# Optimization experiments

Hardware: AMD Instinct MI355X
Metric: run time of the kernel (lower is better)

## Reference

```python
import jax, jax.numpy as jnp
import numpy as np

ROI = 7
EPS = 1e-3


def roi_align(images, frame_idx, boxes_px, oh, ow):
    """Bilinear RoIAlign, sampling_ratio=1 (bin centers), aligned=False.
    images: [F,C,H,W]; frame_idx: [R] int; boxes_px: [R,4] pixel coords.
    Returns [R,oh,ow,C]."""
    F_, C, H, W = images.shape
    R = boxes_px.shape[0]
    x1, y1, x2, y2 = (boxes_px[:, i] for i in range(4))
    bw = (x2 - x1) / ow
    bh = (y2 - y1) / oh
    sx = x1[:, None] + (jnp.arange(ow, dtype=boxes_px.dtype) + 0.5) * bw[:, None]  # [R,ow]
    sy = y1[:, None] + (jnp.arange(oh, dtype=boxes_px.dtype) + 0.5) * bh[:, None]  # [R,oh]
    X = jnp.broadcast_to(sx[:, None, :], (R, oh, ow))
    Y = jnp.broadcast_to(sy[:, :, None], (R, oh, ow))
    valid = (X > -1.0) & (X < W) & (Y > -1.0) & (Y < H)
    x = jnp.clip(X, 0.0, W - 1)
    y = jnp.clip(Y, 0.0, H - 1)
    x0 = jnp.floor(x).astype(jnp.int32)
    y0 = jnp.floor(y).astype(jnp.int32)
    x1i = jnp.minimum(x0 + 1, W - 1)
    y1i = jnp.minimum(y0 + 1, H - 1)
    lx = x - x0
    ly = y - y0
    f = frame_idx[:, None, None]

    def g(yy, xx):
        return images[f, :, yy, xx]  # [R,oh,ow,C]

    v = (g(y0, x0) * ((1 - ly) * (1 - lx))[..., None]
         + g(y0, x1i) * ((1 - ly) * lx)[..., None]
         + g(y1i, x0) * (ly * (1 - lx))[..., None]
         + g(y1i, x1i) * (ly * lx)[..., None])
    return v * valid[..., None].astype(v.dtype)


def bn(x, gamma, beta, mean, var):
    return (x - mean) * jax.lax.rsqrt(var + EPS) * gamma + beta


def setup_inputs() -> dict:
    key = jax.random.key(0)
    ks = jax.random.split(key, 12)
    F_, C, H, W = 64, 256, 40, 40
    N, K = 512, 8
    HID, D = 512, 512
    images = jax.random.normal(ks[0], (F_, C, H, W), jnp.float32)
    kf_indices = jax.random.randint(ks[1], (N, K), 0, F_, jnp.int32)
    u = jax.random.uniform(ks[2], (N, K, 4), jnp.float32)
    x1 = u[..., 0] * 0.6
    y1 = u[..., 1] * 0.6
    x2 = jnp.minimum(x1 + 0.2 + u[..., 2] * 0.2, 1.0)
    y2 = jnp.minimum(y1 + 0.2 + u[..., 3] * 0.2, 1.0)
    boxes = jnp.stack([x1, y1, x2, y2], axis=-1)
    fan1 = C * ROI * ROI
    w1 = jax.random.normal(ks[3], (HID, C, ROI, ROI), jnp.float32) * np.float32(np.sqrt(2.0 / fan1))
    b1 = jnp.zeros((HID,), jnp.float32)
    w2 = jax.random.normal(ks[4], (D, HID), jnp.float32) * np.float32(np.sqrt(2.0 / HID))
    b2 = jnp.zeros((D,), jnp.float32)
    g1 = jnp.ones((HID,), jnp.float32)
    bt1 = jnp.zeros((HID,), jnp.float32)
    m1 = jax.random.normal(ks[5], (HID,), jnp.float32) * 0.1
    v1 = 0.5 + jax.random.uniform(ks[6], (HID,), jnp.float32)
    g2 = jnp.ones((D,), jnp.float32)
    bt2 = jnp.zeros((D,), jnp.float32)
    m2 = jax.random.normal(ks[7], (D,), jnp.float32) * 0.1
    v2 = 0.5 + jax.random.uniform(ks[8], (D,), jnp.float32)
    return {"images": images, "kf_indices": kf_indices, "boxes": boxes,
            "w1": w1, "b1": b1, "g1": g1, "bt1": bt1, "m1": m1, "v1": v1,
            "w2": w2, "b2": b2, "g2": g2, "bt2": bt2, "m2": m2, "v2": v2}


def reference(images, kf_indices, boxes, w1, b1, g1, bt1, m1, v1, w2, b2, g2, bt2, m2, v2):
    F_, C, H, W = images.shape
    N, K = kf_indices.shape
    scale = jnp.asarray([W, H, W, H], images.dtype)
    boxes_px = (boxes * scale).reshape(N * K, 4)
    fidx = kf_indices.reshape(-1)
    roi = roi_align(images, fidx, boxes_px, ROI, ROI)        # [R,7,7,C]
    # conv1 with kernel == roi_region collapses spatial dims -> dense GEMM
    h = jnp.einsum('rhwc,ochw->ro', roi, w1) + b1            # [R,HID]
    h = jax.nn.relu(bn(h, g1, bt1, m1, v1))
    h = h @ w2.T + b2                                        # [R,D]
    h = jax.nn.relu(bn(h, g2, bt2, m2, v2))
    nodes = jnp.max(h.reshape(N, K, -1), axis=1)             # max-aggr over keyframes
    return nodes
```

## Files before the change

kernel.cpp:

```cpp
#include <hip/hip_runtime.h>


typedef __bf16 bf16x8 __attribute__((ext_vector_type(8)));
typedef float f32x4 __attribute__((ext_vector_type(4)));
typedef ushort us8v __attribute__((ext_vector_type(8)));

#define BN_EPS 1e-3f

__device__ __forceinline__ ushort f2bf(float f) {
  union { float f; unsigned u; } v; v.f = f;
  unsigned r = (v.u + 0x7FFFu + ((v.u >> 16) & 1u)) >> 16;
  return (ushort)r;
}
__device__ __forceinline__ float bf2f(ushort b) {
  union { unsigned u; float f; } v; v.u = ((unsigned)b) << 16;
  return v.f;
}
__device__ __forceinline__ void async16(const void* g, void* l) {
  __builtin_amdgcn_global_load_lds((const __attribute__((address_space(1))) void*)g,
                                   (__attribute__((address_space(3))) void*)l, 16, 0, 0);
}

__global__ __launch_bounds__(256, 6) void prep_kernel(const float* __restrict__ img,
                                                      ushort* __restrict__ imgTb,
                                                      const float* __restrict__ w1,
                                                      ushort* __restrict__ w1b,
                                                      const float* __restrict__ w2,
                                                      ushort* __restrict__ w2b,
                                                      const int* __restrict__ kf,
                                                      int* __restrict__ perm) {
  __shared__ __align__(16) char smem[26368];
  const int b = blockIdx.x;
  const int tid = threadIdx.x;
  int tIdx = -1, oIdx = -1;
  if (b < 2307) {
    int q = b / 3, r = b - q * 3;
    if (r < 2) tIdx = q * 2 + r; else oIdx = q;
  } else {
    tIdx = 1538 + (b - 2307);
  }
  if (tIdx >= 0) {
    ushort* lds = (ushort*)smem;
    const int f = tIdx >> 5, rem = tIdx & 31;
    const int cg = rem >> 2, ps = rem & 3;
    const float* src = img + (size_t)f * 409600 + (size_t)(cg * 32) * 1600 + ps * 400;
    for (int i = tid; i < 3200; i += 256) {
      int ch = i / 100, pos = i - ch * 100;
      float4 v = *(const float4*)(src + (size_t)ch * 1600 + pos * 4);
      ushort4 o;
      o.x = f2bf(v.x); o.y = f2bf(v.y); o.z = f2bf(v.z); o.w = f2bf(v.w);
      *(ushort4*)(&lds[ch * 412 + pos * 4]) = o;
    }
    __syncthreads();
    ushort* dst = imgTb + ((size_t)f * 1600 + ps * 400) * 256 + cg * 32;
    for (int e = tid; e < 1600; e += 256) {
      int p = e >> 2, q = e & 3;
      us8v o;
#pragma unroll
      for (int k = 0; k < 8; ++k) o[k] = lds[(q * 8 + k) * 412 + p];
      *(us8v*)(dst + (size_t)p * 256 + q * 8) = o;
    }
  } else if (oIdx < 512) {
    ushort* t = (ushort*)smem;
    const int o = oIdx;
    const float* src = w1 + (size_t)o * 12544;
    for (int j = tid; j < 12544; j += 256) {
      int c = j / 49, p = j - c * 49;
      t[p * 260 + c] = f2bf(src[j]);
    }
    __syncthreads();
    ushort* dst = w1b + (size_t)o * 12544;
    for (int k0 = tid * 8; k0 < 12544; k0 += 2048) {
      int p = k0 >> 8, c = k0 & 255;
      ushort4 a = *(const ushort4*)(&t[p * 260 + c]);
      ushort4 d = *(const ushort4*)(&t[p * 260 + c + 4]);
      us8v o8;
      o8[0] = a.x; o8[1] = a.y; o8[2] = a.z; o8[3] = a.w;
      o8[4] = d.x; o8[5] = d.y; o8[6] = d.z; o8[7] = d.w;
      *(us8v*)(dst + k0) = o8;
    }
  } else if (oIdx < 768) {
    const int o2 = oIdx - 512;
    const size_t base = (size_t)o2 * 1024 + tid * 4;
    float4 vv = *(const float4*)(w2 + base);
    ushort4 o4;
    o4.x = f2bf(vv.x); o4.y = f2bf(vv.y); o4.z = f2bf(vv.z); o4.w = f2bf(vv.w);
    *(ushort4*)(w2b + base) = o4;
  } else {
    int* cnt = (int*)smem;
    int* base = cnt + 64;
    if (tid < 64) cnt[tid] = 0;
    __syncthreads();
    for (int r = tid; r < 4096; r += 256) atomicAdd(&cnt[kf[r]], 1);
    __syncthreads();
    if (tid == 0) {
      int acc = 0;
      for (int f = 0; f < 64; ++f) { base[f] = acc; acc += cnt[f]; }
    }
    __syncthreads();
    for (int r = tid; r < 4096; r += 256) {
      int p = atomicAdd(&base[kf[r]], 1);
      perm[p] = r;
    }
  }
}

__global__ __launch_bounds__(256) void roi_kernel(const ushort* __restrict__ imgTb,
                                                  const int* __restrict__ kf,
                                                  const float* __restrict__ boxes,
                                                  const int* __restrict__ perm,
                                                  ushort* __restrict__ A) {
  __shared__ int sy0[49], sx0[49], sy1[49], sx1[49];
  __shared__ float sw00[49], sw01[49], sw10[49], sw11[49];
  __shared__ int sf, sr;
  const int tid = threadIdx.x;
  if (tid == 0) {
    int r = perm[((blockIdx.x & 7) << 9) | (blockIdx.x >> 3)];
    sr = r;
    sf = kf[r];
  }
  __syncthreads();
  const int r = sr;
  if (tid < 49) {
    int py = tid / 7, px = tid % 7;
    float x1 = boxes[r * 4 + 0] * 40.f, y1 = boxes[r * 4 + 1] * 40.f;
    float x2 = boxes[r * 4 + 2] * 40.f, y2 = boxes[r * 4 + 3] * 40.f;
    float bw = (x2 - x1) * (1.f / 7.f), bh = (y2 - y1) * (1.f / 7.f);
    float X = x1 + (px + 0.5f) * bw, Y = y1 + (py + 0.5f) * bh;
    bool valid = (X > -1.f) && (X < 40.f) && (Y > -1.f) && (Y < 40.f);
    float x = fminf(fmaxf(X, 0.f), 39.f), y = fminf(fmaxf(Y, 0.f), 39.f);
    float x0f = floorf(x), y0f = floorf(y);
    int x0 = (int)x0f, y0 = (int)y0f;
    int x1i = min(x0 + 1, 39), y1i = min(y0 + 1, 39);
    float lx = x - x0f, ly = y - y0f;
    float vm = valid ? 1.f : 0.f;
    sx0[tid] = x0; sy0[tid] = y0; sx1[tid] = x1i; sy1[tid] = y1i;
    sw00[tid] = (1.f - ly) * (1.f - lx) * vm;
    sw01[tid] = (1.f - ly) * lx * vm;
    sw10[tid] = ly * (1.f - lx) * vm;
    sw11[tid] = ly * lx * vm;
  }
  __syncthreads();
  const int c8 = (tid & 31) * 8;
  const int pq = tid >> 5;
  const ushort* base = imgTb + (size_t)sf * 409600 + c8;
  ushort* outp = A + (size_t)r * 12544 + c8;
  for (int p = pq; p < 49; p += 8) {
    const us8v a = *(const us8v*)(base + (size_t)(sy0[p] * 40 + sx0[p]) * 256);
    const us8v b = *(const us8v*)(base + (size_t)(sy0[p] * 40 + sx1[p]) * 256);
    const us8v c = *(const us8v*)(base + (size_t)(sy1[p] * 40 + sx0[p]) * 256);
    const us8v d = *(const us8v*)(base + (size_t)(sy1[p] * 40 + sx1[p]) * 256);
    float w00 = sw00[p], w01 = sw01[p], w10 = sw10[p], w11 = sw11[p];
    us8v o;
#pragma unroll
    for (int k = 0; k < 8; ++k)
      o[k] = f2bf(bf2f(a[k]) * w00 + bf2f(b[k]) * w01 + bf2f(c[k]) * w10 + bf2f(d[k]) * w11);
    *(us8v*)(outp + (size_t)p * 256) = o;
  }
}

__global__ __launch_bounds__(256, 4) void gemm1_kernel(const ushort* __restrict__ A,
                                                       const ushort* __restrict__ B,
                                                       ushort* __restrict__ P) {
  constexpr int K = 12544;
  constexpr int KS = 1792;
  __shared__ __align__(16) ushort sA[128 * 64];
  __shared__ __align__(16) ushort sB[128 * 64];
  const int tid = threadIdx.x;
  const int lane = tid & 63, wave = tid >> 6;
  const int wm = wave >> 1, wn = wave & 1;
  const int r16 = lane & 15, quad = lane >> 4;
  const int r0 = blockIdx.x * 128, c0 = blockIdx.y * 128;
  const int kStart = blockIdx.z * KS, kEnd = kStart + KS;
  const ushort* Ab = A + (size_t)r0 * K;
  const ushort* Bb = B + (size_t)c0 * K;
  const int row8 = tid >> 3;
  const int koff = (((tid & 7) ^ (row8 & 7))) * 8;
  const int sw = r16 & 7;
  f32x4 acc[4][4] = {};
  for (int kk = kStart; kk < kEnd; kk += 64) {
    __syncthreads();
#pragma unroll
    for (int s = 0; s < 4; ++s)
      async16(Ab + (size_t)(s * 32 + row8) * K + kk + koff, (char*)sA + s * 4096 + tid * 16);
#pragma unroll
    for (int s = 0; s < 4; ++s)
      async16(Bb + (size_t)(s * 32 + row8) * K + kk + koff, (char*)sB + s * 4096 + tid * 16);
    __syncthreads();
#pragma unroll
    for (int h = 0; h < 2; ++h) {
      const int slot = ((h * 4 + quad) ^ sw) * 8;
      bf16x8 af[4], bfr[4];
#pragma unroll
      for (int i = 0; i < 4; ++i)
        af[i] = *(const bf16x8*)(sA + (wm * 64 + i * 16 + r16) * 64 + slot);
#pragma unroll
      for (int j = 0; j < 4; ++j)
        bfr[j] = *(const bf16x8*)(sB + (wn * 64 + j * 16 + r16) * 64 + slot);
#pragma unroll
      for (int i = 0; i < 4; ++i)
#pragma unroll
        for (int j = 0; j < 4; ++j)
          acc[i][j] = __builtin_amdgcn_mfma_f32_16x16x32_bf16(af[i], bfr[j], acc[i][j], 0, 0, 0);
    }
  }
  ushort* Pz = P + ((size_t)blockIdx.z * 4096 + r0) * 512 + c0;
#pragma unroll
  for (int i = 0; i < 4; ++i)
#pragma unroll
    for (int j = 0; j < 4; ++j)
#pragma unroll
      for (int g = 0; g < 4; ++g)
        Pz[(size_t)(wm * 64 + i * 16 + quad * 4 + g) * 512 + (wn * 64 + j * 16 + r16)] =
            f2bf(acc[i][j][g]);
}

__global__ __launch_bounds__(256) void combine_kernel(const ushort* __restrict__ P,
                                                      const float* __restrict__ b1,
                                                      const float* __restrict__ g1,
                                                      const float* __restrict__ bt1,
                                                      const float* __restrict__ m1,
                                                      const float* __restrict__ v1,
                                                      ushort* __restrict__ h1) {
  size_t i = (size_t)blockIdx.x * 256 + threadIdx.x;
  int col = (int)(i & 511);
  float x = 0.f;
#pragma unroll
  for (int z = 0; z < 7; ++z) x += bf2f(P[i + (size_t)z * 2097152]);
  float s = g1[col] * rsqrtf(v1[col] + BN_EPS);
  float val = fmaxf((x + b1[col] - m1[col]) * s + bt1[col], 0.f);
  h1[i] = f2bf(val);
}

__global__ __launch_bounds__(256) void gemm2_kernel(const ushort* __restrict__ A,
                                                    const ushort* __restrict__ B,
                                                    const float* __restrict__ b2,
                                                    const float* __restrict__ g2,
                                                    const float* __restrict__ bt2,
                                                    const float* __restrict__ m2,
                                                    const float* __restrict__ v2,
                                                    float* __restrict__ out) {
  constexpr int K = 512;
  __shared__ __align__(16) ushort sA[64 * 64];
  __shared__ __align__(16) ushort sB[128 * 64];
  __shared__ ushort st[64 * 128];
  const int tid = threadIdx.x;
  const int lane = tid & 63, wave = tid >> 6;
  const int wm = wave >> 1, wn = wave & 1;
  const int r16 = lane & 15, quad = lane >> 4;
  const int r0 = blockIdx.x * 64, c0 = blockIdx.y * 128;
  const ushort* Ab = A + (size_t)r0 * K;
  const ushort* Bb = B + (size_t)c0 * K;
  const int row8 = tid >> 3;
  const int koff = (((tid & 7) ^ (row8 & 7))) * 8;
  const int sw = r16 & 7;
  f32x4 acc[2][4] = {};
  for (int kk = 0; kk < K; kk += 64) {
    __syncthreads();
#pragma unroll
    for (int s = 0; s < 2; ++s)
      async16(Ab + (size_t)(s * 32 + row8) * K + kk + koff, (char*)sA + s * 4096 + tid * 16);
#pragma unroll
    for (int s = 0; s < 4; ++s)
      async16(Bb + (size_t)(s * 32 + row8) * K + kk + koff, (char*)sB + s * 4096 + tid * 16);
    __syncthreads();
#pragma unroll
    for (int h = 0; h < 2; ++h) {
      const int slot = ((h * 4 + quad) ^ sw) * 8;
      bf16x8 af[2], bfr[4];
#pragma unroll
      for (int i = 0; i < 2; ++i)
        af[i] = *(const bf16x8*)(sA + (wm * 32 + i * 16 + r16) * 64 + slot);
#pragma unroll
      for (int j = 0; j < 4; ++j)
        bfr[j] = *(const bf16x8*)(sB + (wn * 64 + j * 16 + r16) * 64 + slot);
#pragma unroll
      for (int i = 0; i < 2; ++i)
#pragma unroll
        for (int j = 0; j < 4; ++j)
          acc[i][j] = __builtin_amdgcn_mfma_f32_16x16x32_bf16(af[i], bfr[j], acc[i][j], 0, 0, 0);
    }
  }
  float ss[4], tt[4], bbv[4];
#pragma unroll
  for (int j = 0; j < 4; ++j) {
    int c = c0 + wn * 64 + j * 16 + r16;
    float s = g2[c] * rsqrtf(v2[c] + BN_EPS);
    ss[j] = s; tt[j] = bt2[c] - m2[c] * s; bbv[j] = b2[c];
  }
#pragma unroll
  for (int i = 0; i < 2; ++i)
#pragma unroll
    for (int j = 0; j < 4; ++j)
#pragma unroll
      for (int g = 0; g < 4; ++g) {
        int rr = wm * 32 + i * 16 + quad * 4 + g;
        int cc = wn * 64 + j * 16 + r16;
        float x = (acc[i][j][g] + bbv[j]) * ss[j] + tt[j];
        st[rr * 128 + cc] = f2bf(fmaxf(x, 0.f));
      }
  __syncthreads();
  for (int e = tid; e < 1024; e += 256) {
    int gg = e >> 7, cc = e & 127;
    float m = 0.f;
#pragma unroll
    for (int k = 0; k < 8; ++k) m = fmaxf(m, bf2f(st[(gg * 8 + k) * 128 + cc]));
    out[(size_t)(r0 / 8 + gg) * 512 + c0 + cc] = m;
  }
}

extern "C" void kernel_launch(void* const* d_in, const int* in_sizes, int n_in,
                              void* d_out, int out_size, void* d_ws, size_t ws_size,
                              hipStream_t stream) {
  (void)in_sizes; (void)n_in; (void)out_size; (void)ws_size;
  const float* images = (const float*)d_in[0];
  const int* kf      = (const int*)d_in[1];
  const float* boxes = (const float*)d_in[2];
  const float* w1    = (const float*)d_in[3];
  const float* b1    = (const float*)d_in[4];
  const float* g1    = (const float*)d_in[5];
  const float* bt1   = (const float*)d_in[6];
  const float* m1    = (const float*)d_in[7];
  const float* v1    = (const float*)d_in[8];
  const float* w2    = (const float*)d_in[9];
  const float* b2    = (const float*)d_in[10];
  const float* g2    = (const float*)d_in[11];
  const float* bt2   = (const float*)d_in[12];
  const float* m2    = (const float*)d_in[13];
  const float* v2    = (const float*)d_in[14];
  float* out = (float*)d_out;

  char* ws = (char*)d_ws;
  ushort* Abuf  = (ushort*)(ws + 0);
  ushort* w1b   = (ushort*)(ws + 102760448);
  ushort* w2b   = (ushort*)(ws + 115605504);
  ushort* imgTb = (ushort*)(ws + 116129792);
  ushort* P     = (ushort*)(ws + 116129792);
  ushort* h1    = (ushort*)(ws + 149684224);
  int*    perm  = (int*)(ws + 168558592);

  hipLaunchKernelGGL(prep_kernel, dim3(2817), dim3(256), 0, stream,
                     images, imgTb, w1, w1b, w2, w2b, kf, perm);
  hipLaunchKernelGGL(roi_kernel, dim3(4096), dim3(256), 0, stream, imgTb, kf, boxes, perm, Abuf);
  hipLaunchKernelGGL(gemm1_kernel, dim3(32, 4, 7), dim3(256), 0, stream, Abuf, w1b, P);
  hipLaunchKernelGGL(combine_kernel, dim3(8192), dim3(256), 0, stream, P, b1, g1, bt1, m1, v1, h1);
  hipLaunchKernelGGL(gemm2_kernel, dim3(64, 4), dim3(256), 0, stream, h1, w2b, b2, g2, bt2, m2, v2, out);
}
```

Measured before the change: 324.7 us.

## Fuse image bf16 conversion into RoIAlign with per-frame LDS-resident channel slices

```diff
diff --git a/kernel.cpp b/kernel.cpp
--- a/kernel.cpp
+++ b/kernel.cpp
@@ -21,55 +21,25 @@
                                    (__attribute__((address_space(3))) void*)l, 16, 0, 0);
 }
 
-__global__ __launch_bounds__(256, 6) void prep_kernel(const float* __restrict__ img,
-                                                      ushort* __restrict__ imgTb,
-                                                      const float* __restrict__ w1,
-                                                      ushort* __restrict__ w1b,
-                                                      const float* __restrict__ w2,
-                                                      ushort* __restrict__ w2b,
-                                                      const int* __restrict__ kf,
-                                                      int* __restrict__ perm) {
-  __shared__ __align__(16) char smem[26368];
+__global__ __launch_bounds__(256) void prep_kernel(const float* __restrict__ w1,
+                                                   ushort* __restrict__ w1b,
+                                                   const float* __restrict__ w2,
+                                                   ushort* __restrict__ w2b,
+                                                   const int* __restrict__ kf,
+                                                   int* __restrict__ perm,
+                                                   int* __restrict__ fstart) {
+  __shared__ __align__(16) char smem[25480];
   const int b = blockIdx.x;
   const int tid = threadIdx.x;
-  int tIdx = -1, oIdx = -1;
-  if (b < 2307) {
-    int q = b / 3, r = b - q * 3;
-    if (r < 2) tIdx = q * 2 + r; else oIdx = q;
-  } else {
-    tIdx = 1538 + (b - 2307);
-  }
-  if (tIdx >= 0) {
-    ushort* lds = (ushort*)smem;
-    const int f = tIdx >> 5, rem = tIdx & 31;
-    const int cg = rem >> 2, ps = rem & 3;
-    const float* src = img + (size_t)f * 409600 + (size_t)(cg * 32) * 1600 + ps * 400;
-    for (int i = tid; i < 3200; i += 256) {
-      int ch = i / 100, pos = i - ch * 100;
-      float4 v = *(const float4*)(src + (size_t)ch * 1600 + pos * 4);
-      ushort4 o;
-      o.x = f2bf(v.x); o.y = f2bf(v.y); o.z = f2bf(v.z); o.w = f2bf(v.w);
-      *(ushort4*)(&lds[ch * 412 + pos * 4]) = o;
-    }
-    __syncthreads();
-    ushort* dst = imgTb + ((size_t)f * 1600 + ps * 400) * 256 + cg * 32;
-    for (int e = tid; e < 1600; e += 256) {
-      int p = e >> 2, q = e & 3;
-      us8v o;
-#pragma unroll
-      for (int k = 0; k < 8; ++k) o[k] = lds[(q * 8 + k) * 412 + p];
-      *(us8v*)(dst + (size_t)p * 256 + q * 8) = o;
-    }
-  } else if (oIdx < 512) {
+  if (b < 512) {
     ushort* t = (ushort*)smem;
-    const int o = oIdx;
-    const float* src = w1 + (size_t)o * 12544;
+    const float* src = w1 + (size_t)b * 12544;
     for (int j = tid; j < 12544; j += 256) {
       int c = j / 49, p = j - c * 49;
       t[p * 260 + c] = f2bf(src[j]);
     }
     __syncthreads();
-    ushort* dst = w1b + (size_t)o * 12544;
+    ushort* dst = w1b + (size_t)b * 12544;
     for (int k0 = tid * 8; k0 < 12544; k0 += 2048) {
       int p = k0 >> 8, c = k0 & 255;
       ushort4 a = *(const ushort4*)(&t[p * 260 + c]);
@@ -79,8 +49,8 @@
       o8[4] = d.x; o8[5] = d.y; o8[6] = d.z; o8[7] = d.w;
       *(us8v*)(dst + k0) = o8;
     }
-  } else if (oIdx < 768) {
-    const int o2 = oIdx - 512;
+  } else if (b < 768) {
+    const int o2 = b - 512;
     const size_t base = (size_t)o2 * 1024 + tid * 4;
     float4 vv = *(const float4*)(w2 + base);
     ushort4 o4;
@@ -95,7 +65,8 @@
     __syncthreads();
     if (tid == 0) {
       int acc = 0;
-      for (int f = 0; f < 64; ++f) { base[f] = acc; acc += cnt[f]; }
+      for (int f = 0; f < 64; ++f) { base[f] = acc; fstart[f] = acc; acc += cnt[f]; }
+      fstart[64] = acc;
     }
     __syncthreads();
     for (int r = tid; r < 4096; r += 256) {
@@ -105,57 +76,53 @@
   }
 }
 
-__global__ __launch_bounds__(256) void roi_kernel(const ushort* __restrict__ imgTb,
-                                                  const int* __restrict__ kf,
-                                                  const float* __restrict__ boxes,
-                                                  const int* __restrict__ perm,
-                                                  ushort* __restrict__ A) {
-  __shared__ int sy0[49], sx0[49], sy1[49], sx1[49];
-  __shared__ float sw00[49], sw01[49], sw10[49], sw11[49];
-  __shared__ int sf, sr;
+__global__ __launch_bounds__(512) void roi_fused_kernel(const float* __restrict__ img,
+                                                        const float* __restrict__ boxes,
+                                                        const int* __restrict__ perm,
+                                                        const int* __restrict__ fstart,
+                                                        ushort* __restrict__ A) {
+  __shared__ ushort lds[32 * 1604];
   const int tid = threadIdx.x;
-  if (tid == 0) {
-    int r = perm[((blockIdx.x & 7) << 9) | (blockIdx.x >> 3)];
-    sr = r;
-    sf = kf[r];
+  const int f = blockIdx.x >> 3, cg = blockIdx.x & 7;
+  const float* src = img + (size_t)f * 409600 + (size_t)(cg * 32) * 1600;
+  for (int i = tid; i < 12800; i += 512) {
+    int ch = i / 400, pos = i - ch * 400;
+    float4 v = *(const float4*)(src + (size_t)ch * 1600 + pos * 4);
+    ushort4 o;
+    o.x = f2bf(v.x); o.y = f2bf(v.y); o.z = f2bf(v.z); o.w = f2bf(v.w);
+    *(ushort4*)(&lds[ch * 1604 + pos * 4]) = o;
   }
   __syncthreads();
-  const int r = sr;
-  if (tid < 49) {
-    int py = tid / 7, px = tid % 7;
-    float x1 = boxes[r * 4 + 0] * 40.f, y1 = boxes[r * 4 + 1] * 40.f;
-    float x2 = boxes[r * 4 + 2] * 40.f, y2 = boxes[r * 4 + 3] * 40.f;
-    float bw = (x2 - x1) * (1.f / 7.f), bh = (y2 - y1) * (1.f / 7.f);
-    float X = x1 + (px + 0.5f) * bw, Y = y1 + (py + 0.5f) * bh;
-    bool valid = (X > -1.f) && (X < 40.f) && (Y > -1.f) && (Y < 40.f);
-    float x = fminf(fmaxf(X, 0.f), 39.f), y = fminf(fmaxf(Y, 0.f), 39.f);
-    float x0f = floorf(x), y0f = floorf(y);
-    int x0 = (int)x0f, y0 = (int)y0f;
-    int x1i = min(x0 + 1, 39), y1i = min(y0 + 1, 39);
-    float lx = x - x0f, ly = y - y0f;
-    float vm = valid ? 1.f : 0.f;
-    sx0[tid] = x0; sy0[tid] = y0; sx1[tid] = x1i; sy1[tid] = y1i;
-    sw00[tid] = (1.f - ly) * (1.f - lx) * vm;
-    sw01[tid] = (1.f - ly) * lx * vm;
-    sw10[tid] = ly * (1.f - lx) * vm;
-    sw11[tid] = ly * lx * vm;
-  }
-  __syncthreads();
-  const int c8 = (tid & 31) * 8;
-  const int pq = tid >> 5;
-  const ushort* base = imgTb + (size_t)sf * 409600 + c8;
-  ushort* outp = A + (size_t)r * 12544 + c8;
-  for (int p = pq; p < 49; p += 8) {
-    const us8v a = *(const us8v*)(base + (size_t)(sy0[p] * 40 + sx0[p]) * 256);
-    const us8v b = *(const us8v*)(base + (size_t)(sy0[p] * 40 + sx1[p]) * 256);
-    const us8v c = *(const us8v*)(base + (size_t)(sy1[p] * 40 + sx0[p]) * 256);
-    const us8v d = *(const us8v*)(base + (size_t)(sy1[p] * 40 + sx1[p]) * 256);
-    float w00 = sw00[p], w01 = sw01[p], w10 = sw10[p], w11 = sw11[p];
-    us8v o;
-#pragma unroll
-    for (int k = 0; k < 8; ++k)
-      o[k] = f2bf(bf2f(a[k]) * w00 + bf2f(b[k]) * w01 + bf2f(c[k]) * w10 + bf2f(d[k]) * w11);
-    *(us8v*)(outp + (size_t)p * 256) = o;
+  const int s0 = fstart[f], s1 = fstart[f + 1];
+  ushort* Abase = A + cg * 32;
+  for (int idx = s0; idx < s1; ++idx) {
+    const int r = perm[idx];
+    const float bx1 = boxes[r * 4 + 0] * 40.f, by1 = boxes[r * 4 + 1] * 40.f;
+    const float bx2 = boxes[r * 4 + 2] * 40.f, by2 = boxes[r * 4 + 3] * 40.f;
+    const float bw = (bx2 - bx1) * (1.f / 7.f), bh = (by2 - by1) * (1.f / 7.f);
+    ushort* outp = Abase + (size_t)r * 12544;
+    for (int it = tid; it < 1568; it += 512) {
+      const int p = it >> 5, ch = it & 31;
+      const int py = p / 7, px = p - py * 7;
+      const float X = bx1 + (px + 0.5f) * bw, Y = by1 + (py + 0.5f) * bh;
+      const bool valid = (X > -1.f) && (X < 40.f) && (Y > -1.f) && (Y < 40.f);
+      const float x = fminf(fmaxf(X, 0.f), 39.f), y = fminf(fmaxf(Y, 0.f), 39.f);
+      const float x0f = floorf(x), y0f = floorf(y);
+      const int x0 = (int)x0f, y0 = (int)y0f;
+      const int x1i = min(x0 + 1, 39), y1i = min(y0 + 1, 39);
+      const float lx = x - x0f, ly = y - y0f;
+      const float vm = valid ? 1.f : 0.f;
+      const float w00 = (1.f - ly) * (1.f - lx) * vm;
+      const float w01 = (1.f - ly) * lx * vm;
+      const float w10 = ly * (1.f - lx) * vm;
+      const float w11 = ly * lx * vm;
+      const ushort* row = &lds[ch * 1604];
+      const float a = bf2f(row[y0 * 40 + x0]);
+      const float b = bf2f(row[y0 * 40 + x1i]);
+      const float c = bf2f(row[y1i * 40 + x0]);
+      const float d = bf2f(row[y1i * 40 + x1i]);
+      outp[p * 256 + ch] = f2bf(a * w00 + b * w01 + c * w10 + d * w11);
+    }
   }
 }
 
@@ -334,14 +301,15 @@
   ushort* Abuf  = (ushort*)(ws + 0);
   ushort* w1b   = (ushort*)(ws + 102760448);
   ushort* w2b   = (ushort*)(ws + 115605504);
-  ushort* imgTb = (ushort*)(ws + 116129792);
   ushort* P     = (ushort*)(ws + 116129792);
   ushort* h1    = (ushort*)(ws + 149684224);
   int*    perm  = (int*)(ws + 168558592);
-
-  hipLaunchKernelGGL(prep_kernel, dim3(2817), dim3(256), 0, stream,
-                     images, imgTb, w1, w1b, w2, w2b, kf, perm);
-  hipLaunchKernelGGL(roi_kernel, dim3(4096), dim3(256), 0, stream, imgTb, kf, boxes, perm, Abuf);
+  int*    fstart= (int*)(ws + 168574976);
+
+  hipLaunchKernelGGL(prep_kernel, dim3(769), dim3(256), 0, stream,
+                     w1, w1b, w2, w2b, kf, perm, fstart);
+  hipLaunchKernelGGL(roi_fused_kernel, dim3(512), dim3(512), 0, stream,
+                     images, boxes, perm, fstart, Abuf);
   hipLaunchKernelGGL(gemm1_kernel, dim3(32, 4, 7), dim3(256), 0, stream, Abuf, w1b, P);
   hipLaunchKernelGGL(combine_kernel, dim3(8192), dim3(256), 0, stream, P, b1, g1, bt1, m1, v1, h1);
   hipLaunchKernelGGL(gemm2_kernel, dim3(64, 4), dim3(256), 0, stream, h1, w2b, b2, g2, bt2, m2, v2, out);
```

Result: slower. 426.3 us (+31.3%).
